# Performance work log

Measured on AMD Instinct MI355X. Metric: run time of the kernel, lower is better.

The kernel has to match this reference:

```python
import jax, jax.numpy as jnp
import numpy as np

V, T, E, H, L, B = 50257, 1024, 1024, 16, 12, 4
HD = E // H
FF = 4 * E
EPS = 1e-5


def layer_norm(x, g, b):
    m = jnp.mean(x, axis=-1, keepdims=True)
    v = jnp.mean((x - m) ** 2, axis=-1, keepdims=True)
    return (x - m) * jax.lax.rsqrt(v + EPS) * g + b


def setup_inputs() -> dict:
    key = jax.random.key(0)
    ks = jax.random.split(key, 24)
    s = 0.02
    inp = {
        'idx': jax.random.randint(ks[0], (B, T), 0, V),
        'targets': jax.random.randint(ks[1], (B, T), 0, V),
        'tok_emb': jax.random.normal(ks[2], (V, E), jnp.float32) * s,
        'pos_emb': jax.random.normal(ks[3], (T, E), jnp.float32) * s,
        'Wq': jax.random.normal(ks[4], (L, E, H, HD), jnp.float32) * s,
        'Wk': jax.random.normal(ks[5], (L, E, H, HD), jnp.float32) * s,
        'Wv': jax.random.normal(ks[6], (L, E, H, HD), jnp.float32) * s,
        'Wo': jax.random.normal(ks[7], (L, E, E), jnp.float32) * s,
        'bo': jnp.zeros((L, E), jnp.float32),
        'ln1_g': jnp.ones((L, E), jnp.float32),
        'ln1_b': jnp.zeros((L, E), jnp.float32),
        'ln2_g': jnp.ones((L, E), jnp.float32),
        'ln2_b': jnp.zeros((L, E), jnp.float32),
        'W1': jax.random.normal(ks[8], (L, E, FF), jnp.float32) * s,
        'b1': jnp.zeros((L, FF), jnp.float32),
        'W2': jax.random.normal(ks[9], (L, FF, E), jnp.float32) * s,
        'b2': jnp.zeros((L, E), jnp.float32),
        'lnf_g': jnp.ones((E,), jnp.float32),
        'lnf_b': jnp.zeros((E,), jnp.float32),
        'Whead': jax.random.normal(ks[10], (E, V), jnp.float32) * s,
        'bhead': jnp.zeros((V,), jnp.float32),
    }
    return inp


def forward(idx, targets, tok_emb, pos_emb, Wq, Wk, Wv, Wo, bo, ln1_g, ln1_b,
            ln2_g, ln2_b, W1, b1, W2, b2, lnf_g, lnf_b, Whead, bhead):
    Bc, Tc = idx.shape
    x = tok_emb[idx] + pos_emb[:Tc]  # [B,T,E]
    scale = HD ** -0.5
    causal = jnp.tril(jnp.ones((Tc, Tc), bool))
    for l in range(L):
        h = layer_norm(x, ln1_g[l], ln1_b[l])
        q = jnp.einsum('bte,ehd->bthd', h, Wq[l])
        k = jnp.einsum('bte,ehd->bthd', h, Wk[l])
        v = jnp.einsum('bte,ehd->bthd', h, Wv[l])
        wei = jnp.einsum('bqhd,bkhd->bhqk', q, k) * scale
        wei = jnp.where(causal, wei, -jnp.inf)
        wei = jax.nn.softmax(wei, axis=-1)
        att = jnp.einsum('bhqk,bkhd->bqhd', wei, v).reshape(Bc, Tc, E)
        x = x + att @ Wo[l] + bo[l]
        h = layer_norm(x, ln2_g[l], ln2_b[l])
        # torch nn.GELU default is exact (erf) gelu
        ff = jax.nn.gelu(h @ W1[l] + b1[l], approximate=False) @ W2[l] + b2[l]
        x = x + ff
    x = layer_norm(x, lnf_g, lnf_b)
    logits = x @ Whead + bhead  # [B,T,V]
    logp = jax.nn.log_softmax(logits, axis=-1)
    nll = -jnp.take_along_axis(logp, targets[..., None], axis=-1)[..., 0]
    loss = jnp.mean(nll)
    return logits, loss


def reference(idx, targets, tok_emb, pos_emb, Wq, Wk, Wv, Wo, bo, ln1_g, ln1_b,
              ln2_g, ln2_b, W1, b1, W2, b2, lnf_g, lnf_b, Whead, bhead):
    return forward(idx, targets, tok_emb, pos_emb, Wq, Wk, Wv, Wo, bo, ln1_g,
                   ln1_b, ln2_g, ln2_b, W1, b1, W2, b2, lnf_g, lnf_b, Whead, bhead)
```

## Files before the change

kernel.cpp:

```cpp
#include <hip/hip_runtime.h>
#include <cstdint>
#include <cstddef>

typedef unsigned short u16;
typedef __bf16 bf16x8 __attribute__((ext_vector_type(8)));
typedef float f32x4 __attribute__((ext_vector_type(4)));
typedef unsigned short u16x8 __attribute__((ext_vector_type(8)));
typedef unsigned short u16x4 __attribute__((ext_vector_type(4)));

constexpr int cV  = 50257;
constexpr int cVp = 50432;
constexpr int cNT = cVp / 256;
constexpr int cT  = 1024;
constexpr int cE  = 1024;
constexpr int cL  = 12;
constexpr int cFF = 4096;
constexpr int cBT = 4096;

__device__ __forceinline__ u16 f2bf(float f) {
  union { float f; unsigned u; } x; x.f = f;
  unsigned r = x.u + 0x7fffu + ((x.u >> 16) & 1u);
  return (u16)(r >> 16);
}

__device__ __forceinline__ void gload16(const void* g, void* l) {
  __builtin_amdgcn_global_load_lds(
      (const __attribute__((address_space(1))) void*)g,
      (__attribute__((address_space(3))) void*)l, 16, 0, 0);
}

__device__ __forceinline__ int swzoff(int row, int chunk) {
  return ((chunk ^ (row & 7) ^ ((row >> 3) & 7)) << 4);
}

__device__ __forceinline__ int xcd_swz(int id, int nwg) {
  if ((nwg & 7) == 0) { const int q = nwg >> 3; return (id & 7) * q + (id >> 3); }
  return id;
}

__global__ __launch_bounds__(256) void k_embed(const int* __restrict__ idx,
    const float* __restrict__ tok, const float* __restrict__ pos,
    float* __restrict__ x) {
  const int row = blockIdx.x;
  const int t = row & (cT - 1);
  const int tk = idx[row];
  const float4* tv = (const float4*)(tok + (size_t)tk * cE);
  const float4* pv = (const float4*)(pos + (size_t)t * cE);
  float4* xv = (float4*)(x + (size_t)row * cE);
  const int i = threadIdx.x;
  float4 a = tv[i];
  float4 p = pv[i];
  a.x += p.x; a.y += p.y; a.z += p.z; a.w += p.w;
  xv[i] = a;
}

__global__ __launch_bounds__(256) void k_ln(const float* __restrict__ x,
    const float* __restrict__ gw, const float* __restrict__ bw,
    u16* __restrict__ out) {
  const int row = blockIdx.x;
  const int t = threadIdx.x;
  const float4 v = ((const float4*)(x + (size_t)row * cE))[t];
  float s1 = v.x + v.y + v.z + v.w;
  float s2 = v.x * v.x + v.y * v.y + v.z * v.z + v.w * v.w;
  #pragma unroll
  for (int off = 32; off; off >>= 1) {
    s1 += __shfl_xor(s1, off);
    s2 += __shfl_xor(s2, off);
  }
  __shared__ float red[8];
  const int wid = t >> 6;
  if ((t & 63) == 0) { red[wid] = s1; red[4 + wid] = s2; }
  __syncthreads();
  s1 = red[0] + red[1] + red[2] + red[3];
  s2 = red[4] + red[5] + red[6] + red[7];
  const float mean = s1 * (1.0f / cE);
  const float var = s2 * (1.0f / cE) - mean * mean;
  const float rs = rsqrtf(var + 1e-5f);
  const float4 g4 = ((const float4*)gw)[t];
  const float4 b4 = ((const float4*)bw)[t];
  u16x4 o;
  o[0] = f2bf((v.x - mean) * rs * g4.x + b4.x);
  o[1] = f2bf((v.y - mean) * rs * g4.y + b4.y);
  o[2] = f2bf((v.z - mean) * rs * g4.z + b4.z);
  o[3] = f2bf((v.w - mean) * rs * g4.w + b4.w);
  *(u16x4*)(out + (size_t)row * cE + t * 4) = o;
}

__global__ __launch_bounds__(256) void k_cvt_t(const float* __restrict__ src,
    u16* __restrict__ dst, int K, int Nsrc, size_t sstride, size_t dstride) {
  __shared__ float tile[32][65];
  const float* s = src + blockIdx.z * sstride;
  u16* d = dst + blockIdx.z * dstride;
  const int n0 = blockIdx.x * 64, k0 = blockIdx.y * 32;
  const int t = threadIdx.x;
  #pragma unroll
  for (int p = 0; p < 2; ++p) {
    const int li = p * 256 + t;
    const int k = li >> 4;
    const int n4 = (li & 15) * 4;
    const float* sp = s + (size_t)(k0 + k) * Nsrc + n0 + n4;
    if ((n0 + n4 + 3 < Nsrc) && ((((size_t)(k0 + k) * Nsrc + n0 + n4) & 3) == 0)) {
      const float4 f = *(const float4*)sp;
      tile[k][n4] = f.x; tile[k][n4 + 1] = f.y;
      tile[k][n4 + 2] = f.z; tile[k][n4 + 3] = f.w;
    } else {
      #pragma unroll
      for (int i = 0; i < 4; ++i)
        tile[k][n4 + i] = (n0 + n4 + i < Nsrc) ? sp[i] : 0.0f;
    }
  }
  __syncthreads();
  #pragma unroll
  for (int p = 0; p < 2; ++p) {
    const int si = p * 256 + t;
    const int n = si >> 3;
    const int k4 = (si & 7) * 4;
    u16x4 o;
    #pragma unroll
    for (int i = 0; i < 4; ++i) o[i] = f2bf(tile[k4 + i][n]);
    *(u16x4*)(d + (size_t)(n0 + n) * K + k0 + k4) = o;
  }
}

template<int EPI>
__global__ __launch_bounds__(512, 4) void k_gemm2(
    const u16* __restrict__ A, const u16* __restrict__ Bt,
    const float* __restrict__ bias, u16* __restrict__ obf,
    float* __restrict__ of, int K, int Nout, int ntile, int mt,
    float* __restrict__ pm, float* __restrict__ ps) {
  __shared__ __align__(16) char smem[49152];
  const int tid = threadIdx.x;
  const int lane = tid & 63;
  const int wid = tid >> 6;
  const int wg = (int)blockIdx.x;
  const int bm = wg % mt;
  const int bn = wg / mt;
  const int wm = wid >> 2, wn = wid & 3;
  const int l15 = lane & 15, lg = lane >> 4;

  f32x4 acc[4][4];
  #pragma unroll
  for (int i = 0; i < 4; ++i)
    #pragma unroll
    for (int j = 0; j < 4; ++j) { f32x4 z = {0.f,0.f,0.f,0.f}; acc[i][j] = z; }

  const u16* Ab = A + (size_t)(bm * 128) * K;
  const u16* Bb = Bt + (size_t)(bn * 256) * K;
  const int nt = K >> 5;

  auto stage = [&](int t) {
    char* buf = smem + ((t & 1) ? 24576 : 0);
    const int kt = t << 5;
    {
      const int r = tid >> 2, c = tid & 3;
      gload16(Ab + (size_t)r * K + kt + ((c ^ ((r >> 1) & 3)) << 3),
              buf + tid * 16);
    }
    #pragma unroll
    for (int p = 0; p < 2; ++p) {
      const int L = p * 512 + tid;
      const int r = L >> 2, c = L & 3;
      gload16(Bb + (size_t)r * K + kt + ((c ^ ((r >> 1) & 3)) << 3),
              buf + 8192 + L * 16);
    }
  };

  stage(0);
  for (int t = 0; t < nt; ++t) {
    __syncthreads();
    if (t + 1 < nt) stage(t + 1);
    char* cs = smem + ((t & 1) ? 24576 : 0);
    const char* csB = cs + 8192;
    bf16x8 af[4], bfr[4];
    #pragma unroll
    for (int mi = 0; mi < 4; ++mi) {
      const int row = wm * 64 + mi * 16 + l15;
      af[mi] = *(const bf16x8*)(cs + row * 64 + ((lg ^ ((row >> 1) & 3)) << 4));
    }
    #pragma unroll
    for (int ni = 0; ni < 4; ++ni) {
      const int row = wn * 64 + ni * 16 + l15;
      bfr[ni] = *(const bf16x8*)(csB + row * 64 + ((lg ^ ((row >> 1) & 3)) << 4));
    }
    #pragma unroll
    for (int ni = 0; ni < 4; ++ni)
      #pragma unroll
      for (int mi = 0; mi < 4; ++mi)
        acc[mi][ni] = __builtin_amdgcn_mfma_f32_16x16x32_bf16(af[mi], bfr[ni], acc[mi][ni], 0, 0, 0);
  }

  if constexpr (EPI == 3) {
    __syncthreads();
    float* pb = (float*)smem;
    #pragma unroll
    for (int mi = 0; mi < 4; ++mi) {
      const int grow = bm * 128 + wm * 64 + mi * 16 + lg * 4;
      float rm[4];
      #pragma unroll
      for (int r = 0; r < 4; ++r) rm[r] = -1e30f;
      #pragma unroll
      for (int ni = 0; ni < 4; ++ni) {
        const int gcol = bn * 256 + wn * 64 + ni * 16 + l15;
        const bool ok = gcol < Nout;
        const float bb = ok ? bias[gcol] : 0.0f;
        #pragma unroll
        for (int r = 0; r < 4; ++r) {
          const float v = ok ? (acc[mi][ni][r] + bb) : -1e30f;
          acc[mi][ni][r] = v;
          if (ok) of[(size_t)(grow + r) * Nout + gcol] = v;
          rm[r] = fmaxf(rm[r], v);
        }
      }
      #pragma unroll
      for (int r = 0; r < 4; ++r) {
        float m = rm[r];
        #pragma unroll
        for (int off = 1; off < 16; off <<= 1) m = fmaxf(m, __shfl_xor(m, off));
        float s = 0.f;
        #pragma unroll
        for (int ni = 0; ni < 4; ++ni) s += __expf(acc[mi][ni][r] - m);
        #pragma unroll
        for (int off = 1; off < 16; off <<= 1) s += __shfl_xor(s, off);
        if (l15 == 0) {
          const int lrow = wm * 64 + mi * 16 + lg * 4 + r;
          pb[(lrow * 4 + wn) * 2] = m;
          pb[(lrow * 4 + wn) * 2 + 1] = s;
        }
      }
    }
    __syncthreads();
    if (tid < 128) {
      float m = -1e30f, s = 0.f;
      #pragma unroll
      for (int q = 0; q < 4; ++q) {
        const float m2 = pb[(tid * 4 + q) * 2];
        const float s2 = pb[(tid * 4 + q) * 2 + 1];
        const float M = fmaxf(m, m2);
        s = s * __expf(m - M) + s2 * __expf(m2 - M);
        m = M;
      }
      const size_t grow = (size_t)(bm * 128 + tid);
      pm[grow * ntile + bn] = m;
      ps[grow * ntile + bn] = s;
    }
  } else {
    #pragma unroll
    for (int mi = 0; mi < 4; ++mi) {
      const int grow = bm * 128 + wm * 64 + mi * 16 + lg * 4;
      #pragma unroll
      for (int ni = 0; ni < 4; ++ni) {
        const int gcol = bn * 256 + wn * 64 + ni * 16 + l15;
        #pragma unroll
        for (int r = 0; r < 4; ++r) {
          const float a = acc[mi][ni][r];
          if constexpr (EPI == 0) {
            obf[(size_t)(gcol >> 10) * 4194304 + (size_t)(grow + r) * 1024 + (gcol & 1023)] = f2bf(a);
          } else {
            const float gv = a + bias[gcol];
            obf[(size_t)(grow + r) * Nout + gcol] = f2bf(0.5f * gv * (1.0f + erff(gv * 0.70710678118f)));
          }
        }
      }
    }
  }
}

__global__ __launch_bounds__(256) void k_gemm_s(
    const u16* __restrict__ A, const u16* __restrict__ Bt,
    const float* __restrict__ bias, float* __restrict__ of,
    int K, int Nout, int mt) {
  __shared__ __align__(16) char smem[49152];
  const int tid = threadIdx.x;
  const int lane = tid & 63;
  const int wid = tid >> 6;
  const int wg = xcd_swz((int)blockIdx.x, (int)gridDim.x);
  const int bm = wg % mt;
  const int bn = wg / mt;
  const int wr = wid >> 1, wc = wid & 1;
  const int l15 = lane & 15, lg = lane >> 4;

  f32x4 acc[2][4];
  #pragma unroll
  for (int i = 0; i < 2; ++i)
    #pragma unroll
    for (int j = 0; j < 4; ++j) { f32x4 z = {0.f,0.f,0.f,0.f}; acc[i][j] = z; }

  const u16* Ab = A + (size_t)(bm * 64) * K;
  const u16* Bb = Bt + (size_t)(bn * 128) * K;
  const int nt = K >> 6;

  auto stage = [&](int t, char* buf) {
    const int kt = (t < nt ? t : nt - 1) << 6;
    #pragma unroll
    for (int p = 0; p < 2; ++p) {
      const int L = p * 256 + tid;
      const int row = L >> 3, cc = L & 7;
      gload16(Ab + (size_t)row * K + kt + ((cc ^ (row & 7)) << 3), buf + L * 16);
    }
    #pragma unroll
    for (int p = 0; p < 4; ++p) {
      const int L = p * 256 + tid;
      const int row = L >> 3, cc = L & 7;
      gload16(Bb + (size_t)row * K + kt + ((cc ^ (row & 7)) << 3), buf + 8192 + L * 16);
    }
  };
  stage(0, smem);
  stage(1, smem + 24576);

  for (int t = 0; t < nt; ++t) {
    char* cs = smem + ((t & 1) ? 24576 : 0);
    const char* csB = cs + 8192;
    asm volatile("s_waitcnt vmcnt(6)" ::: "memory");
    __builtin_amdgcn_s_barrier();

    bf16x8 af[2][2], bfr[4][2];
    #pragma unroll
    for (int mi = 0; mi < 2; ++mi) {
      const int row = wr * 32 + mi * 16 + l15;
      #pragma unroll
      for (int kk = 0; kk < 2; ++kk)
        af[mi][kk] = *(const bf16x8*)(cs + row * 128 + (((kk * 4 + lg) ^ (row & 7)) << 4));
    }
    #pragma unroll
    for (int ni = 0; ni < 4; ++ni) {
      const int row = wc * 64 + ni * 16 + l15;
      #pragma unroll
      for (int kk = 0; kk < 2; ++kk)
        bfr[ni][kk] = *(const bf16x8*)(csB + row * 128 + (((kk * 4 + lg) ^ (row & 7)) << 4));
    }
    __builtin_amdgcn_sched_barrier(0);
    __builtin_amdgcn_s_setprio(1);
    #pragma unroll
    for (int ni = 0; ni < 4; ++ni)
      #pragma unroll
      for (int mi = 0; mi < 2; ++mi)
        acc[mi][ni] = __builtin_amdgcn_mfma_f32_16x16x32_bf16(af[mi][0], bfr[ni][0], acc[mi][ni], 0, 0, 0);
    __builtin_amdgcn_s_setprio(0);
    __builtin_amdgcn_sched_barrier(0);
    asm volatile("s_waitcnt lgkmcnt(0)" ::: "memory");
    __builtin_amdgcn_sched_barrier(0);
    __builtin_amdgcn_s_barrier();

    stage(t + 2, cs);
    __builtin_amdgcn_sched_barrier(0);
    __builtin_amdgcn_s_setprio(1);
    #pragma unroll
    for (int ni = 0; ni < 4; ++ni)
      #pragma unroll
      for (int mi = 0; mi < 2; ++mi)
        acc[mi][ni] = __builtin_amdgcn_mfma_f32_16x16x32_bf16(af[mi][1], bfr[ni][1], acc[mi][ni], 0, 0, 0);
    __builtin_amdgcn_s_setprio(0);
    __builtin_amdgcn_sched_barrier(0);
  }
  asm volatile("s_waitcnt vmcnt(0)" ::: "memory");

  #pragma unroll
  for (int mi = 0; mi < 2; ++mi) {
    const int grow = bm * 64 + wr * 32 + mi * 16 + lg * 4;
    #pragma unroll
    for (int ni = 0; ni < 4; ++ni) {
      const int gcol = bn * 128 + wc * 64 + ni * 16 + l15;
      #pragma unroll
      for (int r = 0; r < 4; ++r)
        of[(size_t)(grow + r) * Nout + gcol] += acc[mi][ni][r] + bias[gcol];
    }
  }
}

__global__ __launch_bounds__(256) void k_gemm_legacy3(
    const u16* __restrict__ A, const float* __restrict__ B0,
    const float* __restrict__ bias, float* __restrict__ of,
    int M, int N, int K) {
  __shared__ u16 Al[128 * 32];
  __shared__ u16 Bl[32 * 128];
  const int tid = threadIdx.x;
  const int lane = tid & 63;
  const int wid = tid >> 6;
  const int bn = blockIdx.x;
  const int bm = blockIdx.y;
  const int wr = wid >> 1, wc = wid & 1;
  const int l15 = lane & 15, lg = lane >> 4;
  f32x4 acc[4][4];
  #pragma unroll
  for (int i = 0; i < 4; ++i)
    #pragma unroll
    for (int j = 0; j < 4; ++j) { f32x4 z = {0.f,0.f,0.f,0.f}; acc[i][j] = z; }
  const u16* Abase = A + (size_t)(bm * 128) * K;
  const int ar0 = tid >> 2;
  const int ac0 = (tid & 3) * 8;
  const int brow = tid >> 3;
  const int bc0 = (tid & 7) * 16;
  for (int kt = 0; kt < K; kt += 32) {
    *(u16x8*)(Al + ar0 * 32 + ac0) =
        *(const u16x8*)(Abase + (size_t)ar0 * K + kt + ac0);
    *(u16x8*)(Al + (ar0 + 64) * 32 + ac0) =
        *(const u16x8*)(Abase + (size_t)(ar0 + 64) * K + kt + ac0);
    {
      const float* bsrc = B0 + (size_t)(kt + brow) * N + bn * 128 + bc0;
      alignas(16) u16 tmp[16];
      const int colbase = bn * 128 + bc0;
      #pragma unroll
      for (int q = 0; q < 16; ++q)
        tmp[q] = f2bf((colbase + q < N) ? bsrc[q] : 0.0f);
      *(u16x8*)(Bl + brow * 128 + bc0) = *(const u16x8*)tmp;
      *(u16x8*)(Bl + brow * 128 + bc0 + 8) = *(const u16x8*)(tmp + 8);
    }
    __syncthreads();
    bf16x8 af[4];
    #pragma unroll
    for (int mi = 0; mi < 4; ++mi)
      af[mi] = *(const bf16x8*)(Al + (wr * 64 + mi * 16 + l15) * 32 + lg * 8);
    #pragma unroll
    for (int ni = 0; ni < 4; ++ni) {
      u16x8 tv;
      #pragma unroll
      for (int i = 0; i < 8; ++i)
        tv[i] = Bl[(lg * 8 + i) * 128 + wc * 64 + ni * 16 + l15];
      const bf16x8 bfr = __builtin_bit_cast(bf16x8, tv);
      #pragma unroll
      for (int mi = 0; mi < 4; ++mi)
        acc[mi][ni] = __builtin_amdgcn_mfma_f32_16x16x32_bf16(af[mi], bfr, acc[mi][ni], 0, 0, 0);
    }
    __syncthreads();
  }
  #pragma unroll
  for (int mi = 0; mi < 4; ++mi) {
    const int grow = bm * 128 + wr * 64 + mi * 16 + lg * 4;
    #pragma unroll
    for (int ni = 0; ni < 4; ++ni) {
      const int gcol = bn * 128 + wc * 64 + ni * 16 + l15;
      #pragma unroll
      for (int r = 0; r < 4; ++r)
        if (gcol < N) of[(size_t)(grow + r) * N + gcol] = acc[mi][ni][r] + bias[gcol];
    }
  }
}

__global__ __launch_bounds__(512, 2) void k_attn(
    const u16* __restrict__ qg, const u16* __restrict__ kg,
    const u16* __restrict__ vg, u16* __restrict__ og) {
  __shared__ u16 Kl[64 * 64];
  __shared__ u16 Vt[64 * 64];
  __shared__ u16 Pl[8][16 * 64];
  const int tid = threadIdx.x;
  const int lane = tid & 63;
  const int w = tid >> 6;
  const int bx = blockIdx.x;
  const int bh = blockIdx.y;
  const int b = bh >> 4, h = bh & 15;
  const int l15 = lane & 15, lg = lane >> 4;
  char* KlB = (char*)Kl;
  char* VtB = (char*)Vt;
  char* PlB = (char*)(Pl[w]);

  const int qwr = bx * 128 + w * 16;
  const int diagkt = qwr >> 6;
  const size_t qrow0 = (size_t)b * cT + qwr;
  bf16x8 aq[2];
  #pragma unroll
  for (int c = 0; c < 2; ++c)
    aq[c] = *(const bf16x8*)(qg + (qrow0 + l15) * cE + h * 64 + c * 32 + lg * 8);

  f32x4 acco[4];
  #pragma unroll
  for (int j = 0; j < 4; ++j) { f32x4 z = {0.f,0.f,0.f,0.f}; acco[j] = z; }
  float mrun[4], lrun[4];
  #pragma unroll
  for (int r = 0; r < 4; ++r) { mrun[r] = -1e30f; lrun[r] = 0.f; }

  const int ktmax = 2 * bx + 1;
  for (int kt = 0; kt <= ktmax; ++kt) {
    const size_t krow0 = (size_t)b * cT + kt * 64;
    {
      const int rr = tid >> 3, c8 = (tid & 7) * 8;
      *(u16x8*)(KlB + rr * 128 + swzoff(rr, c8 >> 3)) =
          *(const u16x8*)(kg + (krow0 + rr) * cE + h * 64 + c8);
      const u16x8 vv = *(const u16x8*)(vg + (krow0 + rr) * cE + h * 64 + c8);
      #pragma unroll
      for (int i = 0; i < 8; ++i)
        *(u16*)(VtB + (c8 + i) * 128 + swzoff(c8 + i, rr >> 3) + (rr & 7) * 2) = vv[i];
    }
    __syncthreads();

    if (kt <= diagkt) {
      f32x4 s[4];
      #pragma unroll
      for (int j = 0; j < 4; ++j) { f32x4 z = {0.f,0.f,0.f,0.f}; s[j] = z; }
      #pragma unroll
      for (int c = 0; c < 2; ++c) {
        #pragma unroll
        for (int j = 0; j < 4; ++j) {
          const int n = j * 16 + l15;
          const bf16x8 kb2 = *(const bf16x8*)(KlB + n * 128 + swzoff(n, c * 4 + lg));
          s[j] = __builtin_amdgcn_mfma_f32_16x16x32_bf16(aq[c], kb2, s[j], 0, 0, 0);
        }
      }

      float sv[4][4];
      const bool diag = (kt == diagkt);
      #pragma unroll
      for (int j = 0; j < 4; ++j)
        #pragma unroll
        for (int r = 0; r < 4; ++r) {
          float xs = s[j][r] * 0.125f;
          if (diag && (kt * 64 + j * 16 + l15) > (qwr + lg * 4 + r)) xs = -1e30f;
          sv[j][r] = xs;
        }

      float corr[4];
      #pragma unroll
      for (int r = 0; r < 4; ++r) {
        float mx = fmaxf(fmaxf(sv[0][r], sv[1][r]), fmaxf(sv[2][r], sv[3][r]));
        #pragma unroll
        for (int off = 1; off < 16; off <<= 1) mx = fmaxf(mx, __shfl_xor(mx, off));
        const float mnew = fmaxf(mrun[r], mx);
        corr[r] = __expf(mrun[r] - mnew);
        float rs = 0.f;
        #pragma unroll
        for (int j = 0; j < 4; ++j) {
          const float p = __expf(sv[j][r] - mnew);
          sv[j][r] = p;
          rs += p;
        }
        #pragma unroll
        for (int off = 1; off < 16; off <<= 1) rs += __shfl_xor(rs, off);
        lrun[r] = lrun[r] * corr[r] + rs;
        mrun[r] = mnew;
      }

      #pragma unroll
      for (int j = 0; j < 4; ++j)
        #pragma unroll
        for (int r = 0; r < 4; ++r) {
          const int qr = lg * 4 + r, kc = j * 16 + l15;
          *(u16*)(PlB + qr * 128 + swzoff(qr, kc >> 3) + (kc & 7) * 2) = f2bf(sv[j][r]);
          acco[j][r] *= corr[r];
        }

      #pragma unroll
      for (int c = 0; c < 2; ++c) {
        const bf16x8 pa = *(const bf16x8*)(PlB + l15 * 128 + swzoff(l15, c * 4 + lg));
        #pragma unroll
        for (int j = 0; j < 4; ++j) {
          const int n = j * 16 + l15;
          const bf16x8 vb2 = *(const bf16x8*)(VtB + n * 128 + swzoff(n, c * 4 + lg));
          acco[j] = __builtin_amdgcn_mfma_f32_16x16x32_bf16(pa, vb2, acco[j], 0, 0, 0);
        }
      }
    }
    __syncthreads();
  }

  #pragma unroll
  for (int j = 0; j < 4; ++j)
    #pragma unroll
    for (int r = 0; r < 4; ++r)
      og[(qrow0 + lg * 4 + r) * cE + h * 64 + j * 16 + l15] = f2bf(acco[j][r] / lrun[r]);
}

__global__ __launch_bounds__(256) void k_nll2(const float* __restrict__ pm,
    const float* __restrict__ ps, const float* __restrict__ logits,
    const int* __restrict__ tgt, float* __restrict__ nll, int NT) {
  const int row = blockIdx.x * 4 + (threadIdx.x >> 6);
  const int lane = threadIdx.x & 63;
  float m = -1e30f, s = 0.f;
  for (int i = lane; i < NT; i += 64) {
    const float m2 = pm[(size_t)row * NT + i];
    const float s2 = ps[(size_t)row * NT + i];
    const float M = fmaxf(m, m2);
    s = s * __expf(m - M) + s2 * __expf(m2 - M);
    m = M;
  }
  #pragma unroll
  for (int off = 1; off < 64; off <<= 1) {
    const float m2 = __shfl_xor(m, off);
    const float s2 = __shfl_xor(s, off);
    const float M = fmaxf(m, m2);
    s = s * __expf(m - M) + s2 * __expf(m2 - M);
    m = M;
  }
  if (lane == 0)
    nll[row] = logf(s) + m - logits[(size_t)row * cV + tgt[row]];
}

__global__ __launch_bounds__(256) void k_nll(const float* __restrict__ logits,
    const int* __restrict__ tgt, float* __restrict__ nll) {
  const int row = blockIdx.x;
  const float* lp = logits + (size_t)row * cV;
  const int t = threadIdx.x;
  __shared__ float red[8];
  const int wid = t >> 6, lane = t & 63;
  float mx = -1e30f;
  for (int i = t; i < cV; i += 256) mx = fmaxf(mx, lp[i]);
  #pragma unroll
  for (int off = 32; off; off >>= 1) mx = fmaxf(mx, __shfl_xor(mx, off));
  if (lane == 0) red[wid] = mx;
  __syncthreads();
  mx = fmaxf(fmaxf(red[0], red[1]), fmaxf(red[2], red[3]));
  float s = 0.f;
  for (int i = t; i < cV; i += 256) s += __expf(lp[i] - mx);
  #pragma unroll
  for (int off = 32; off; off >>= 1) s += __shfl_xor(s, off);
  if (lane == 0) red[4 + wid] = s;
  __syncthreads();
  if (t == 0) {
    s = red[4] + red[5] + red[6] + red[7];
    nll[row] = logf(s) + mx - lp[tgt[row]];
  }
}

__global__ __launch_bounds__(256) void k_loss(const float* __restrict__ nll,
    float* __restrict__ out) {
  const int t = threadIdx.x;
  float s = 0.f;
  for (int i = t; i < cBT; i += 256) s += nll[i];
  #pragma unroll
  for (int off = 32; off; off >>= 1) s += __shfl_xor(s, off);
  __shared__ float red[4];
  if ((t & 63) == 0) red[t >> 6] = s;
  __syncthreads();
  if (t == 0) out[0] = (red[0] + red[1] + red[2] + red[3]) * (1.0f / cBT);
}

extern "C" void kernel_launch(void* const* d_in, const int* in_sizes, int n_in,
                              void* d_out, int out_size, void* d_ws, size_t ws_size,
                              hipStream_t stream) {
  const int*   idx  = (const int*)d_in[0];
  const int*   tgt  = (const int*)d_in[1];
  const float* tok  = (const float*)d_in[2];
  const float* pos  = (const float*)d_in[3];
  const float* Wq   = (const float*)d_in[4];
  const float* Wk   = (const float*)d_in[5];
  const float* Wv   = (const float*)d_in[6];
  const float* Wo   = (const float*)d_in[7];
  const float* bo   = (const float*)d_in[8];
  const float* ln1g = (const float*)d_in[9];
  const float* ln1b = (const float*)d_in[10];
  const float* ln2g = (const float*)d_in[11];
  const float* ln2b = (const float*)d_in[12];
  const float* W1   = (const float*)d_in[13];
  const float* b1   = (const float*)d_in[14];
  const float* W2   = (const float*)d_in[15];
  const float* b2   = (const float*)d_in[16];
  const float* lnfg = (const float*)d_in[17];
  const float* lnfb = (const float*)d_in[18];
  const float* Wh   = (const float*)d_in[19];
  const float* bh   = (const float*)d_in[20];

  char* ob = (char*)d_out;
  float* x    = (float*)ob;
  u16* hb     = (u16*)(ob + (16u << 20));
  u16* qb     = (u16*)(ob + (24u << 20));
  u16* kb     = (u16*)(ob + (32u << 20));
  u16* vb     = (u16*)(ob + (40u << 20));
  u16* abuf   = (u16*)(ob + (48u << 20));
  u16* fbuf   = (u16*)(ob + (56u << 20));
  u16* W3T    = (u16*)(ob + (128u << 20));
  u16* WoT    = (u16*)(ob + (200u << 20));
  u16* W1T    = (u16*)(ob + (224u << 20));
  u16* W2T    = (u16*)(ob + (320u << 20));
  u16* hf     = (u16*)d_ws;
  float* nll  = (float*)((char*)d_ws + 8388608);
  u16* WheadT = (u16*)((char*)d_ws + 8404992);
  const size_t whead_end = 8404992u + (size_t)cVp * cE * 2u;
  float* pmax = (float*)((char*)d_ws + whead_end);
  float* psum = (float*)((char*)d_ws + whead_end + (size_t)cBT * cNT * 4);
  const size_t ws_need = whead_end + 2u * (size_t)cBT * cNT * 4;
  const bool fast_head = ws_size >= ws_need;

  float* logits = (float*)d_out;
  float* loss = logits + (size_t)cBT * cV;

  const dim3 blk(256);
  const size_t e2 = (size_t)cE * cE, ef = (size_t)cE * cFF;

  k_cvt_t<<<dim3(16, 32, cL), blk, 0, stream>>>(Wq, W3T,          cE, cE, e2, 3 * e2);
  k_cvt_t<<<dim3(16, 32, cL), blk, 0, stream>>>(Wk, W3T + e2,     cE, cE, e2, 3 * e2);
  k_cvt_t<<<dim3(16, 32, cL), blk, 0, stream>>>(Wv, W3T + 2 * e2, cE, cE, e2, 3 * e2);
  k_cvt_t<<<dim3(16, 32, cL), blk, 0, stream>>>(Wo, WoT, cE, cE, e2, e2);
  k_cvt_t<<<dim3(64, 32, cL), blk, 0, stream>>>(W1, W1T, cE, cFF, ef, ef);
  k_cvt_t<<<dim3(16, 128, cL), blk, 0, stream>>>(W2, W2T, cFF, cE, ef, ef);
  if (fast_head)
    k_cvt_t<<<dim3(cVp / 64, 32, 1), blk, 0, stream>>>(Wh, WheadT, cE, cV, 0, 0);

  k_embed<<<dim3(cBT), blk, 0, stream>>>(idx, tok, pos, x);
  for (int l = 0; l < cL; ++l) {
    k_ln<<<dim3(cBT), blk, 0, stream>>>(x, ln1g + l * cE, ln1b + l * cE, hb);
    k_gemm2<0><<<dim3(32 * 12), dim3(512), 0, stream>>>(hb, W3T + l * 3 * e2,
        nullptr, qb, nullptr, cE, 3072, 0, 32, nullptr, nullptr);
    k_attn<<<dim3(8, 64), dim3(512), 0, stream>>>(qb, kb, vb, abuf);
    k_gemm_s<<<dim3(512), blk, 0, stream>>>(abuf, WoT + l * e2, bo + l * cE, x, cE, cE, 64);
    k_ln<<<dim3(cBT), blk, 0, stream>>>(x, ln2g + l * cE, ln2b + l * cE, hb);
    k_gemm2<2><<<dim3(32 * 16), dim3(512), 0, stream>>>(hb, W1T + l * ef,
        b1 + l * cFF, fbuf, nullptr, cE, cFF, 0, 32, nullptr, nullptr);
    k_gemm_s<<<dim3(512), blk, 0, stream>>>(fbuf, W2T + l * ef, b2 + l * cE, x, cFF, cE, 64);
  }
  k_ln<<<dim3(cBT), blk, 0, stream>>>(x, lnfg, lnfb, hf);
  if (fast_head) {
    k_gemm2<3><<<dim3(32 * cNT), dim3(512), 0, stream>>>(hf, WheadT, bh,
        nullptr, logits, cE, cV, cNT, 32, pmax, psum);
    k_nll2<<<dim3(cBT / 4), blk, 0, stream>>>(pmax, psum, logits, tgt, nll, cNT);
  } else {
    k_gemm_legacy3<<<dim3(393, 32), blk, 0, stream>>>(hf, Wh, bh, logits, cBT, cV, cE);
    k_nll<<<dim3(cBT), blk, 0, stream>>>(logits, tgt, nll);
  }
  k_loss<<<dim3(1), blk, 0, stream>>>(nll, loss);
}
```

Measured before the change: 4.108 ms.

## Process two query groups per attention block to reuse staged K/V tiles

Each attention block now handles 256 query rows, as two 128-row groups per wave, instead of 128. Every K/V tile staged into shared memory is reused by both groups, which halves the grid and the global K/V loads and transposes per query. The cost is more registers per thread (two sets of accumulators and Q fragments), only 256 blocks, and worse causal load imbalance since the lower group idles on the later tiles.

```diff
diff --git a/kernel.cpp b/kernel.cpp
--- a/kernel.cpp
+++ b/kernel.cpp
@@ -441,7 +441,7 @@
     const u16* __restrict__ vg, u16* __restrict__ og) {
   __shared__ u16 Kl[64 * 64];
   __shared__ u16 Vt[64 * 64];
-  __shared__ u16 Pl[8][16 * 64];
+  __shared__ u16 Pl[8][2][16 * 64];
   const int tid = threadIdx.x;
   const int lane = tid & 63;
   const int w = tid >> 6;
@@ -451,24 +451,31 @@
   const int l15 = lane & 15, lg = lane >> 4;
   char* KlB = (char*)Kl;
   char* VtB = (char*)Vt;
-  char* PlB = (char*)(Pl[w]);
-
-  const int qwr = bx * 128 + w * 16;
-  const int diagkt = qwr >> 6;
-  const size_t qrow0 = (size_t)b * cT + qwr;
-  bf16x8 aq[2];
-  #pragma unroll
-  for (int c = 0; c < 2; ++c)
-    aq[c] = *(const bf16x8*)(qg + (qrow0 + l15) * cE + h * 64 + c * 32 + lg * 8);
-
-  f32x4 acco[4];
-  #pragma unroll
-  for (int j = 0; j < 4; ++j) { f32x4 z = {0.f,0.f,0.f,0.f}; acco[j] = z; }
-  float mrun[4], lrun[4];
-  #pragma unroll
-  for (int r = 0; r < 4; ++r) { mrun[r] = -1e30f; lrun[r] = 0.f; }
-
-  const int ktmax = 2 * bx + 1;
+
+  int qwr[2], diagkt[2];
+  size_t qrow0[2];
+  bf16x8 aq[2][2];
+  #pragma unroll
+  for (int g = 0; g < 2; ++g) {
+    qwr[g] = bx * 256 + g * 128 + w * 16;
+    diagkt[g] = qwr[g] >> 6;
+    qrow0[g] = (size_t)b * cT + qwr[g];
+    #pragma unroll
+    for (int c = 0; c < 2; ++c)
+      aq[g][c] = *(const bf16x8*)(qg + (qrow0[g] + l15) * cE + h * 64 + c * 32 + lg * 8);
+  }
+
+  f32x4 acco[2][4];
+  float mrun[2][4], lrun[2][4];
+  #pragma unroll
+  for (int g = 0; g < 2; ++g) {
+    #pragma unroll
+    for (int j = 0; j < 4; ++j) { f32x4 z = {0.f,0.f,0.f,0.f}; acco[g][j] = z; }
+    #pragma unroll
+    for (int r = 0; r < 4; ++r) { mrun[g][r] = -1e30f; lrun[g][r] = 0.f; }
+  }
+
+  const int ktmax = 4 * bx + 3;
   for (int kt = 0; kt <= ktmax; ++kt) {
     const size_t krow0 = (size_t)b * cT + kt * 64;
     {
@@ -482,80 +489,87 @@
     }
     __syncthreads();
 
-    if (kt <= diagkt) {
-      f32x4 s[4];
-      #pragma unroll
-      for (int j = 0; j < 4; ++j) { f32x4 z = {0.f,0.f,0.f,0.f}; s[j] = z; }
-      #pragma unroll
-      for (int c = 0; c < 2; ++c) {
-        #pragma unroll
-        for (int j = 0; j < 4; ++j) {
-          const int n = j * 16 + l15;
-          const bf16x8 kb2 = *(const bf16x8*)(KlB + n * 128 + swzoff(n, c * 4 + lg));
-          s[j] = __builtin_amdgcn_mfma_f32_16x16x32_bf16(aq[c], kb2, s[j], 0, 0, 0);
+    #pragma unroll
+    for (int g = 0; g < 2; ++g) {
+      if (kt <= diagkt[g]) {
+        char* PlB = (char*)(Pl[w][g]);
+        f32x4 s[4];
+        #pragma unroll
+        for (int j = 0; j < 4; ++j) { f32x4 z = {0.f,0.f,0.f,0.f}; s[j] = z; }
+        #pragma unroll
+        for (int c = 0; c < 2; ++c) {
+          #pragma unroll
+          for (int j = 0; j < 4; ++j) {
+            const int n = j * 16 + l15;
+            const bf16x8 kb2 = *(const bf16x8*)(KlB + n * 128 + swzoff(n, c * 4 + lg));
+            s[j] = __builtin_amdgcn_mfma_f32_16x16x32_bf16(aq[g][c], kb2, s[j], 0, 0, 0);
+          }
+        }
+
+        float sv[4][4];
+        const bool diag = (kt == diagkt[g]);
+        #pragma unroll
+        for (int j = 0; j < 4; ++j)
+          #pragma unroll
+          for (int r = 0; r < 4; ++r) {
+            float xs = s[j][r] * 0.125f;
+            if (diag && (kt * 64 + j * 16 + l15) > (qwr[g] + lg * 4 + r)) xs = -1e30f;
+            sv[j][r] = xs;
+          }
+
+        float corr[4];
+        #pragma unroll
+        for (int r = 0; r < 4; ++r) {
+          float mx = fmaxf(fmaxf(sv[0][r], sv[1][r]), fmaxf(sv[2][r], sv[3][r]));
+          #pragma unroll
+          for (int off = 1; off < 16; off <<= 1) mx = fmaxf(mx, __shfl_xor(mx, off));
+          const float mnew = fmaxf(mrun[g][r], mx);
+          corr[r] = __expf(mrun[g][r] - mnew);
+          float rs = 0.f;
+          #pragma unroll
+          for (int j = 0; j < 4; ++j) {
+            const float p = __expf(sv[j][r] - mnew);
+            sv[j][r] = p;
+            rs += p;
+          }
+          #pragma unroll
+          for (int off = 1; off < 16; off <<= 1) rs += __shfl_xor(rs, off);
+          lrun[g][r] = lrun[g][r] * corr[r] + rs;
+          mrun[g][r] = mnew;
+        }
+
+        #pragma unroll
+        for (int j = 0; j < 4; ++j)
+          #pragma unroll
+          for (int r = 0; r < 4; ++r) {
+            const int qr = lg * 4 + r, kc = j * 16 + l15;
+            *(u16*)(PlB + qr * 128 + swzoff(qr, kc >> 3) + (kc & 7) * 2) = f2bf(sv[j][r]);
+            acco[g][j][r] *= corr[r];
+          }
+
+        #pragma unroll
+        for (int c = 0; c < 2; ++c) {
+          const bf16x8 pa = *(const bf16x8*)(PlB + l15 * 128 + swzoff(l15, c * 4 + lg));
+          #pragma unroll
+          for (int j = 0; j < 4; ++j) {
+            const int n = j * 16 + l15;
+            const bf16x8 vb2 = *(const bf16x8*)(VtB + n * 128 + swzoff(n, c * 4 + lg));
+            acco[g][j] = __builtin_amdgcn_mfma_f32_16x16x32_bf16(pa, vb2, acco[g][j], 0, 0, 0);
+          }
         }
       }
-
-      float sv[4][4];
-      const bool diag = (kt == diagkt);
-      #pragma unroll
-      for (int j = 0; j < 4; ++j)
-        #pragma unroll
-        for (int r = 0; r < 4; ++r) {
-          float xs = s[j][r] * 0.125f;
-          if (diag && (kt * 64 + j * 16 + l15) > (qwr + lg * 4 + r)) xs = -1e30f;
-          sv[j][r] = xs;
-        }
-
-      float corr[4];
-      #pragma unroll
-      for (int r = 0; r < 4; ++r) {
-        float mx = fmaxf(fmaxf(sv[0][r], sv[1][r]), fmaxf(sv[2][r], sv[3][r]));
-        #pragma unroll
-        for (int off = 1; off < 16; off <<= 1) mx = fmaxf(mx, __shfl_xor(mx, off));
-        const float mnew = fmaxf(mrun[r], mx);
-        corr[r] = __expf(mrun[r] - mnew);
-        float rs = 0.f;
-        #pragma unroll
-        for (int j = 0; j < 4; ++j) {
-          const float p = __expf(sv[j][r] - mnew);
-          sv[j][r] = p;
-          rs += p;
-        }
-        #pragma unroll
-        for (int off = 1; off < 16; off <<= 1) rs += __shfl_xor(rs, off);
-        lrun[r] = lrun[r] * corr[r] + rs;
-        mrun[r] = mnew;
-      }
-
-      #pragma unroll
-      for (int j = 0; j < 4; ++j)
-        #pragma unroll
-        for (int r = 0; r < 4; ++r) {
-          const int qr = lg * 4 + r, kc = j * 16 + l15;
-          *(u16*)(PlB + qr * 128 + swzoff(qr, kc >> 3) + (kc & 7) * 2) = f2bf(sv[j][r]);
-          acco[j][r] *= corr[r];
-        }
-
-      #pragma unroll
-      for (int c = 0; c < 2; ++c) {
-        const bf16x8 pa = *(const bf16x8*)(PlB + l15 * 128 + swzoff(l15, c * 4 + lg));
-        #pragma unroll
-        for (int j = 0; j < 4; ++j) {
-          const int n = j * 16 + l15;
-          const bf16x8 vb2 = *(const bf16x8*)(VtB + n * 128 + swzoff(n, c * 4 + lg));
-          acco[j] = __builtin_amdgcn_mfma_f32_16x16x32_bf16(pa, vb2, acco[j], 0, 0, 0);
-        }
-      }
     }
     __syncthreads();
   }
 
   #pragma unroll
-  for (int j = 0; j < 4; ++j)
-    #pragma unroll
-    for (int r = 0; r < 4; ++r)
-      og[(qrow0 + lg * 4 + r) * cE + h * 64 + j * 16 + l15] = f2bf(acco[j][r] / lrun[r]);
+  for (int g = 0; g < 2; ++g)
+    #pragma unroll
+    for (int j = 0; j < 4; ++j)
+      #pragma unroll
+      for (int r = 0; r < 4; ++r)
+        og[(qrow0[g] + lg * 4 + r) * cE + h * 64 + j * 16 + l15] =
+            f2bf(acco[g][j][r] / lrun[g][r]);
 }
 
 __global__ __launch_bounds__(256) void k_nll2(const float* __restrict__ pm,
@@ -688,7 +702,7 @@
     k_ln<<<dim3(cBT), blk, 0, stream>>>(x, ln1g + l * cE, ln1b + l * cE, hb);
     k_gemm2<0><<<dim3(32 * 12), dim3(512), 0, stream>>>(hb, W3T + l * 3 * e2,
         nullptr, qb, nullptr, cE, 3072, 0, 32, nullptr, nullptr);
-    k_attn<<<dim3(8, 64), dim3(512), 0, stream>>>(qb, kb, vb, abuf);
+    k_attn<<<dim3(4, 64), dim3(512), 0, stream>>>(qb, kb, vb, abuf);
     k_gemm_s<<<dim3(512), blk, 0, stream>>>(abuf, WoT + l * e2, bo + l * cE, x, cE, cE, 64);
     k_ln<<<dim3(cBT), blk, 0, stream>>>(x, ln2g + l * cE, ln2b + l * cE, hb);
     k_gemm2<2><<<dim3(32 * 16), dim3(512), 0, stream>>>(hb, W1T + l * ef,
```

After: 3.961 ms. 3.6% less time.
